# Optimization experiments

Hardware: AMD Instinct MI355X
Metric: run time of the kernel (lower is better)

Reference implementation:

```python
import jax, jax.numpy as jnp
import numpy as np

N = 100000   # nodes
E = 300000   # edges
D = 256      # emb_dim
L = 5        # num_layers
SELF_LOOP_BOND_TYPE = 4
BN_EPS = 1e-5


def setup_inputs() -> dict:
    key = jax.random.key(0)
    ks = jax.random.split(key, 12)
    s = 0.05
    x = jax.random.randint(ks[0], (N, 2), 0, 3)
    edge_index = jax.random.randint(ks[1], (2, E), 0, N)
    edge_attr = jax.random.randint(ks[2], (E, 2), 0, 3)
    x_emb1 = jax.random.normal(ks[3], (120, D), dtype=jnp.float32) * s
    x_emb2 = jax.random.normal(ks[4], (3, D), dtype=jnp.float32) * s
    edge_emb1 = jax.random.normal(ks[5], (L, 6, D), dtype=jnp.float32) * s
    edge_emb2 = jax.random.normal(ks[6], (L, 3, D), dtype=jnp.float32) * s
    W1 = jax.random.normal(ks[7], (L, D, 2 * D), dtype=jnp.float32) * (1.0 / np.sqrt(D))
    b1 = jnp.zeros((L, 2 * D), dtype=jnp.float32)
    W2 = jax.random.normal(ks[8], (L, 2 * D, D), dtype=jnp.float32) * (1.0 / np.sqrt(2 * D))
    b2 = jnp.zeros((L, D), dtype=jnp.float32)
    bn_gamma = jnp.ones((L - 1, D), dtype=jnp.float32)
    bn_beta = jnp.zeros((L - 1, D), dtype=jnp.float32)
    return dict(x=x, edge_index=edge_index, edge_attr=edge_attr,
                x_emb1=x_emb1, x_emb2=x_emb2,
                edge_emb1=edge_emb1, edge_emb2=edge_emb2,
                W1=W1, b1=b1, W2=W2, b2=b2,
                bn_gamma=bn_gamma, bn_beta=bn_beta)


def reference(x, edge_index, edge_attr, x_emb1, x_emb2, edge_emb1, edge_emb2,
              W1, b1, W2, b2, bn_gamma, bn_beta):
    n = x.shape[0]
    loop = jnp.arange(n)
    # add_self_loops: append (i, i) for every node
    src = jnp.concatenate([edge_index[0], loop])  # [E+N]
    dst = jnp.concatenate([edge_index[1], loop])  # [E+N]
    # self-loop edge_attr = (bond_type=4, direction=0)
    self_attr = jnp.concatenate([
        jnp.full((n, 1), SELF_LOOP_BOND_TYPE, dtype=edge_attr.dtype),
        jnp.zeros((n, 1), dtype=edge_attr.dtype)], axis=1)
    ea = jnp.concatenate([edge_attr, self_attr], axis=0)  # [E+N, 2]

    out = x_emb1[x[:, 0]] + x_emb2[x[:, 1]]  # [N, D]
    for l in range(L):
        e_emb = edge_emb1[l][ea[:, 0]] + edge_emb2[l][ea[:, 1]]  # [E+N, D]
        msg = out[src] + e_emb                                   # gather + message
        agg = jax.ops.segment_sum(msg, dst, num_segments=n)      # scatter-add
        h = jax.nn.relu(agg @ W1[l] + b1[l]) @ W2[l] + b2[l]     # GIN MLP
        if l < L - 1:
            mean = h.mean(axis=0)
            var = h.var(axis=0)  # biased var, matches torch BN training
            h = (h - mean) * jax.lax.rsqrt(var + BN_EPS) * bn_gamma[l] + bn_beta[l]
            h = jax.nn.relu(h)
        out = h
    return out
```

## Files before the change

### kernel.cpp

```cpp
#include <hip/hip_runtime.h>

typedef unsigned short u16;
typedef unsigned int u32;

#define DD 256

typedef short  s16x8 __attribute__((ext_vector_type(8)));
typedef short  s16x4 __attribute__((ext_vector_type(4)));
typedef float  f32x4 __attribute__((ext_vector_type(4)));

__device__ __forceinline__ float b2f(u16 u){
  union { u32 i; float f; } c; c.i = ((u32)u) << 16; return c.f;
}
__device__ __forceinline__ u16 f2b(float f){
  union { float f; u32 i; } c; c.f = f;
  u32 b = c.i + 0x7FFFu + ((c.i >> 16) & 1u);
  return (u16)(b >> 16);
}

__global__ void NodeEncoder_72971494359603_kernel(){}

__global__ void probe_dtype(const u32* w, u32* flag){
  if (threadIdx.x == 0 && blockIdx.x == 0){
    int cnt = 0;
    for (int i = 0; i < 256; i++){
      u32 low = w[i] & 0xFFFFu;
      u32 e = (low >> 7) & 0xFFu;
      if (e >= 0x60u && e <= 0x7Eu) cnt++;
    }
    *flag = (cnt >= 192) ? 1u : 0u;
  }
}

__global__ void cvt_in(const void* src, u16* dst, int n, const u32* flag){
  int i = blockIdx.x * 256 + threadIdx.x;
  if (i < n){
    if (*flag){
      dst[i] = ((const u16*)src)[i];
    } else {
      dst[i] = f2b(((const float*)src)[i]);
    }
  }
}

__global__ void store_out(const u16* h, void* dout, int n, const u32* flag){
  int i = blockIdx.x * 256 + threadIdx.x;
  if (i < n){
    if (*flag){
      ((u16*)dout)[i] = h[i];
    } else {
      ((float*)dout)[i] = b2f(h[i]);
    }
  }
}

__global__ void zero_int(int* p, int n){
  int i = blockIdx.x * 256 + threadIdx.x;
  if (i < n) p[i] = 0;
}

__global__ void build_table(const u16* ee1, const u16* ee2, float* TBL){
  int b = blockIdx.x;
  int l = b / 18, c = b % 18, a = c / 3, bb = c % 3;
  int j = threadIdx.x;
  TBL[b * DD + j] = b2f(ee1[(l * 6 + a) * DD + j]) + b2f(ee2[(l * 3 + bb) * DD + j]);
}

__global__ void hist_kernel(const int* dst, int* counts, int E){
  int e = blockIdx.x * 256 + threadIdx.x;
  if (e < E) atomicAdd(&counts[dst[e]], 1);
}

__global__ void scan_sums(const int* counts, int* bsum, int N){
  __shared__ int red[256];
  int tid = threadIdx.x;
  int base = blockIdx.x * 1024;
  int s = 0;
  for (int i = tid; i < 1024; i += 256){
    int g = base + i;
    if (g < N) s += counts[g];
  }
  red[tid] = s;
  __syncthreads();
  for (int off = 128; off > 0; off >>= 1){
    if (tid < off) red[tid] += red[tid + off];
    __syncthreads();
  }
  if (tid == 0) bsum[blockIdx.x] = red[0];
}

__global__ void scan_top(int* bsum, int nb){
  if (threadIdx.x == 0 && blockIdx.x == 0){
    int acc = 0;
    for (int i = 0; i < nb; i++){ int t = bsum[i]; bsum[i] = acc; acc += t; }
  }
}

__global__ void scan_block(const int* counts, const int* bsum,
                           int* offsets, int* cursor, int N){
  __shared__ int tsum[256];
  int b = blockIdx.x;
  int tid = threadIdx.x;
  int base = b * 1024;
  int v0, v1, v2, v3;
  int g = base + tid * 4;
  v0 = (g + 0 < N) ? counts[g + 0] : 0;
  v1 = (g + 1 < N) ? counts[g + 1] : 0;
  v2 = (g + 2 < N) ? counts[g + 2] : 0;
  v3 = (g + 3 < N) ? counts[g + 3] : 0;
  tsum[tid] = v0 + v1 + v2 + v3;
  __syncthreads();
  for (int off = 1; off < 256; off <<= 1){
    int t = (tid >= off) ? tsum[tid - off] : 0;
    __syncthreads();
    tsum[tid] += t;
    __syncthreads();
  }
  int excl = (tid == 0 ? 0 : tsum[tid - 1]) + bsum[b];
  if (g + 0 < N){ offsets[g + 0] = excl; cursor[g + 0] = excl; } excl += v0;
  if (g + 1 < N){ offsets[g + 1] = excl; cursor[g + 1] = excl; } excl += v1;
  if (g + 2 < N){ offsets[g + 2] = excl; cursor[g + 2] = excl; } excl += v2;
  if (g + 3 < N){ offsets[g + 3] = excl; cursor[g + 3] = excl; }
}

__global__ void fill_csr(const int* ei, const int* ea, int* cursor,
                         int* payload, int E){
  int e = blockIdx.x * 256 + threadIdx.x;
  if (e < E){
    int d = ei[E + e];
    int pos = atomicAdd(&cursor[d], 1);
    int a = ea[2 * e], bb = ea[2 * e + 1];
    payload[pos] = ei[e] | ((a * 3 + bb) << 17);
  }
}

__global__ void node_embed(const int* x, const u16* xe1, const u16* xe2,
                           u16* out, int N){
  int idx = blockIdx.x * 256 + threadIdx.x;
  if (idx < N * DD){
    int n = idx >> 8, j = idx & 255;
    int x0 = x[2 * n], x1 = x[2 * n + 1];
    out[idx] = f2b(b2f(xe1[x0 * DD + j]) + b2f(xe2[x1 * DD + j]));
  }
}

__global__ void pack_B(const u16* __restrict__ W0, u16* __restrict__ Wp0, int K, int Nc){
  const u16* W = W0 + (size_t)blockIdx.y * K * Nc;
  u16* Wp = Wp0 + (size_t)blockIdx.y * K * Nc;
  int idx = blockIdx.x * 256 + threadIdx.x;
  int lane = idx & 63;
  int t = idx >> 6;
  int nk = K >> 5;
  int ksub = t % nk, cblk = t / nk;
  if (cblk >= (Nc >> 4)) return;
  int col = cblk * 16 + (lane & 15);
  int krow = ksub * 32 + (lane >> 4) * 8;
  u16* dst = Wp + (size_t)idx * 8;
#pragma unroll
  for (int e = 0; e < 8; e++)
    dst[e] = W[(size_t)(krow + e) * Nc + col];
}

__global__ __launch_bounds__(512, 4)
void layer_fused(const u16* __restrict__ feat, const float* __restrict__ TBL,
                 const int* __restrict__ offsets, const int* __restrict__ counts,
                 const int* __restrict__ payload,
                 const u16* __restrict__ Wp1, const u16* __restrict__ bias1,
                 const u16* __restrict__ Wp2, const u16* __restrict__ bias2,
                 u16* __restrict__ H, float* __restrict__ partial, int npart, int M,
                 const float* __restrict__ sums, const u16* __restrict__ gamma,
                 const u16* __restrict__ beta, float invN, int apply_bn){
  __shared__ __align__(16) u16 As[64 * 256];
  __shared__ __align__(16) u16 Ms[2][64 * 128];
  float* T = (float*)Ms;
  int tid = threadIdx.x, lane = tid & 63, wave = tid >> 6;
  int wr = wave >> 2, wc = wave & 3;
  int row0 = blockIdx.x * 64;
  int lr = lane & 15, hi = lane >> 4;

  for (int i = tid; i < 18 * DD; i += 512) T[i] = TBL[i];
  __syncthreads();

  {
    int c4 = lane * 4;
    float sc[4], sh[4];
    if (apply_bn){
#pragma unroll
      for (int e = 0; e < 4; e++){
        int j = c4 + e;
        float mean = sums[j] * invN;
        float var = sums[DD + j] * invN - mean * mean;
        if (var < 0.f) var = 0.f;
        float scl = rsqrtf(var + 1e-5f) * b2f(gamma[j]);
        sc[e] = scl; sh[e] = b2f(beta[j]) - mean * scl;
      }
    } else {
#pragma unroll
      for (int e = 0; e < 4; e++){ sc[e] = 1.f; sh[e] = 0.f; }
    }
    for (int u = 0; u < 8; u++){
      int r = wave * 8 + u;
      int n = row0 + r; if (n > M - 1) n = M - 1;
      s16x4 sv = *(const s16x4*)(feat + (size_t)n * DD + c4);
      f32x4 tb = *(const f32x4*)(T + 12 * DD + c4);
      float v0 = b2f((u16)sv[0]) * sc[0] + sh[0];
      float v1 = b2f((u16)sv[1]) * sc[1] + sh[1];
      float v2 = b2f((u16)sv[2]) * sc[2] + sh[2];
      float v3 = b2f((u16)sv[3]) * sc[3] + sh[3];
      if (apply_bn){
        v0 = fmaxf(v0, 0.f); v1 = fmaxf(v1, 0.f);
        v2 = fmaxf(v2, 0.f); v3 = fmaxf(v3, 0.f);
      }
      float a0 = v0 + tb[0], a1 = v1 + tb[1], a2 = v2 + tb[2], a3 = v3 + tb[3];
      int e0 = offsets[n], eend = e0 + counts[n];
      for (int e = e0; e < eend; e += 4){
        int nb = eend - e; if (nb > 4) nb = 4;
        int pls[4]; s16x4 rvs[4]; f32x4 tvs[4];
#pragma unroll
        for (int i = 0; i < 4; i++)
          if (i < nb) pls[i] = payload[e + i];
#pragma unroll
        for (int i = 0; i < 4; i++)
          if (i < nb){
            rvs[i] = *(const s16x4*)(feat + (size_t)(pls[i] & 0x1FFFF) * DD + c4);
            tvs[i] = *(const f32x4*)(T + (pls[i] >> 17) * DD + c4);
          }
#pragma unroll
        for (int i = 0; i < 4; i++)
          if (i < nb){
            float w0 = b2f((u16)rvs[i][0]) * sc[0] + sh[0];
            float w1 = b2f((u16)rvs[i][1]) * sc[1] + sh[1];
            float w2 = b2f((u16)rvs[i][2]) * sc[2] + sh[2];
            float w3 = b2f((u16)rvs[i][3]) * sc[3] + sh[3];
            if (apply_bn){
              w0 = fmaxf(w0, 0.f); w1 = fmaxf(w1, 0.f);
              w2 = fmaxf(w2, 0.f); w3 = fmaxf(w3, 0.f);
            }
            a0 += w0 + tvs[i][0];
            a1 += w1 + tvs[i][1];
            a2 += w2 + tvs[i][2];
            a3 += w3 + tvs[i][3];
          }
      }
      s16x4 o;
      o[0] = (short)f2b(a0); o[1] = (short)f2b(a1);
      o[2] = (short)f2b(a2); o[3] = (short)f2b(a3);
      int byteo = r * 512 + ((((lane >> 1) ^ (r & 7)) & 31) << 4) + ((lane & 1) << 3);
      *(s16x4*)((char*)As + byteo) = o;
    }
  }
  __syncthreads();

  f32x4 zero = {0.f, 0.f, 0.f, 0.f};
  f32x4 acc2[2][4];
#pragma unroll
  for (int m = 0; m < 2; m++)
#pragma unroll
    for (int n = 0; n < 4; n++) acc2[m][n] = zero;
  f32x4 acc1[2][2];

  auto G1 = [&](int cc){
#pragma unroll
    for (int m = 0; m < 2; m++)
#pragma unroll
      for (int n = 0; n < 2; n++) acc1[m][n] = zero;
#pragma unroll
    for (int ks = 0; ks < 8; ks++){
      s16x8 af[2];
#pragma unroll
      for (int m = 0; m < 2; m++){
        int arow = wr * 32 + m * 16 + lr;
        af[m] = *(const s16x8*)((const char*)As + arow * 512 +
                                ((ks * 64 + hi * 16) ^ ((arow & 7) << 4)));
      }
#pragma unroll
      for (int n = 0; n < 2; n++){
        int cb = cc * 8 + wc * 2 + n;
        s16x8 bf = *(const s16x8*)(Wp1 + (((size_t)cb * 8 + ks) * 64 + lane) * 8);
        acc1[0][n] = __builtin_amdgcn_mfma_f32_16x16x32_bf16(af[0], bf, acc1[0][n], 0, 0, 0);
        acc1[1][n] = __builtin_amdgcn_mfma_f32_16x16x32_bf16(af[1], bf, acc1[1][n], 0, 0, 0);
      }
    }
  };
  auto WMS = [&](int cc, int buf){
    char* ms = (char*)Ms[buf];
#pragma unroll
    for (int n = 0; n < 2; n++){
      float bv = b2f(bias1[cc * 128 + wc * 32 + n * 16 + lr]);
      int c2 = (wc * 32 + n * 16 + lr) * 2;
#pragma unroll
      for (int m = 0; m < 2; m++)
#pragma unroll
        for (int r = 0; r < 4; r++){
          int mrow = wr * 32 + m * 16 + hi * 4 + r;
          float v = fmaxf(acc1[m][n][r] + bv, 0.f);
          *(u16*)(ms + mrow * 256 + (c2 ^ ((mrow & 7) << 4))) = f2b(v);
        }
    }
  };

  G1(0);
  WMS(0, 0);
  __syncthreads();

#pragma unroll
  for (int c = 0; c < 4; c++){
    const char* ms = (const char*)Ms[c & 1];
#pragma unroll
    for (int ks = 0; ks < 4; ks++){
      s16x8 mf[2];
#pragma unroll
      for (int m = 0; m < 2; m++){
        int mrow = wr * 32 + m * 16 + lr;
        mf[m] = *(const s16x8*)(ms + mrow * 256 +
                                ((ks * 64 + hi * 16) ^ ((mrow & 7) << 4)));
      }
#pragma unroll
      for (int n = 0; n < 4; n++){
        int cb2 = wc * 4 + n;
        s16x8 wf = *(const s16x8*)(Wp2 + (((size_t)cb2 * 16 + c * 4 + ks) * 64 + lane) * 8);
        acc2[0][n] = __builtin_amdgcn_mfma_f32_16x16x32_bf16(mf[0], wf, acc2[0][n], 0, 0, 0);
        acc2[1][n] = __builtin_amdgcn_mfma_f32_16x16x32_bf16(mf[1], wf, acc2[1][n], 0, 0, 0);
      }
    }
    if (c < 3){
      G1(c + 1);
      WMS(c + 1, (c + 1) & 1);
      __syncthreads();
    }
  }

#pragma unroll
  for (int n = 0; n < 4; n++){
    float bv = b2f(bias2[wc * 64 + n * 16 + lr]);
    int c2 = (wc * 64 + n * 16 + lr) * 2;
#pragma unroll
    for (int m = 0; m < 2; m++)
#pragma unroll
      for (int r = 0; r < 4; r++){
        int mrow = wr * 32 + m * 16 + hi * 4 + r;
        *(u16*)((char*)As + mrow * 512 + (c2 ^ ((mrow & 7) << 4))) = f2b(acc2[m][n][r] + bv);
      }
  }
  __syncthreads();

  float s[8], q[8];
#pragma unroll
  for (int e = 0; e < 8; e++){ s[e] = 0.f; q[e] = 0.f; }
  int sl = tid & 31;
#pragma unroll
  for (int p = 0; p < 4; p++){
    int r = p * 16 + (tid >> 5);
    s16x8 v = *(const s16x8*)((const char*)As + r * 512 + ((sl << 4) ^ ((r & 7) << 4)));
    int gr = row0 + r;
    if (gr < M){
      *(s16x8*)(H + (size_t)gr * DD + sl * 8) = v;
      if (partial){
#pragma unroll
        for (int e = 0; e < 8; e++){
          float f = b2f((u16)v[e]);
          s[e] += f; q[e] += f * f;
        }
      }
    }
  }
  if (partial){
#pragma unroll
    for (int e = 0; e < 8; e++){
      s[e] += __shfl_xor(s[e], 32);
      q[e] += __shfl_xor(q[e], 32);
    }
    float* redS = (float*)Ms;
    float* redQ = redS + 8 * 256;
    if (lane < 32){
#pragma unroll
      for (int e = 0; e < 8; e++){
        redS[wave * 256 + sl * 8 + e] = s[e];
        redQ[wave * 256 + sl * 8 + e] = q[e];
      }
    }
    __syncthreads();
    if (tid < 256){
      float a = 0.f, b = 0.f;
#pragma unroll
      for (int w = 0; w < 8; w++){ a += redS[w * 256 + tid]; b += redQ[w * 256 + tid]; }
      partial[(size_t)blockIdx.x * DD + tid] = a;
      partial[(size_t)(npart + blockIdx.x) * DD + tid] = b;
    }
  }
}

__global__ void bn_reduce(const float* __restrict__ partial, float* __restrict__ sums,
                          int npart){
  int b = blockIdx.x, which = b >> 3, jg = b & 7;
  int t = threadIdx.x;
  int j = jg * 32 + (t >> 3);
  int li = t & 7;
  float s = 0.f;
  for (int i = li; i < npart; i += 8)
    s += partial[(size_t)(which * npart + i) * DD + j];
  s += __shfl_xor(s, 1); s += __shfl_xor(s, 2); s += __shfl_xor(s, 4);
  if (li == 0) sums[which * DD + j] = s;
}

extern "C" void kernel_launch(void* const* d_in, const int* in_sizes, int n_in,
                              void* d_out, int out_size, void* d_ws, size_t ws_size,
                              hipStream_t stream){
  (void)n_in; (void)out_size; (void)ws_size;
  const int* x    = (const int*)d_in[0];
  const int* ei   = (const int*)d_in[1];
  const int* ea   = (const int*)d_in[2];
  const void* xe1 = d_in[3];
  const void* xe2 = d_in[4];
  const void* ee1 = d_in[5];
  const void* ee2 = d_in[6];
  const void* W1  = d_in[7];
  const void* b1  = d_in[8];
  const void* W2  = d_in[9];
  const void* b2  = d_in[10];
  const void* gam = d_in[11];
  const void* bet = d_in[12];

  int N = in_sizes[0] / 2;
  int E = in_sizes[1] / 2;
  int NB = (N + 1023) / 1024;
  const int L = 5;
  int nblk = (N + 63) / 64;
  int npart = nblk;

  char* base = (char*)d_ws;
  size_t off = 0;
  u32* flag    = (u32*)(base + off);   off += 256;
  float* TBL   = (float*)(base + off); off += ((size_t)L * 18 * DD * 4 + 255) & ~(size_t)255;
  int* counts  = (int*)(base + off);   off += ((size_t)N * 4 + 255) & ~(size_t)255;
  int* offsets = (int*)(base + off);   off += ((size_t)N * 4 + 255) & ~(size_t)255;
  int* cursor  = (int*)(base + off);   off += ((size_t)N * 4 + 255) & ~(size_t)255;
  int* bsum    = (int*)(base + off);   off += ((size_t)NB * 4 + 255) & ~(size_t)255;
  int* payload = (int*)(base + off);   off += ((size_t)E * 4 + 255) & ~(size_t)255;
  float* part  = (float*)(base + off); off += ((size_t)2 * npart * DD * 4 + 255) & ~(size_t)255;
  float* sums  = (float*)(base + off); off += ((size_t)2 * DD * 4 + 255) & ~(size_t)255;
  u16* wx1  = (u16*)(base + off); off += ((size_t)120 * DD * 2 + 255) & ~(size_t)255;
  u16* wx2  = (u16*)(base + off); off += ((size_t)3 * DD * 2 + 255) & ~(size_t)255;
  u16* wee1 = (u16*)(base + off); off += ((size_t)L * 6 * DD * 2 + 255) & ~(size_t)255;
  u16* wee2 = (u16*)(base + off); off += ((size_t)L * 3 * DD * 2 + 255) & ~(size_t)255;
  u16* wW1  = (u16*)(base + off); off += ((size_t)L * DD * 2 * DD * 2 + 255) & ~(size_t)255;
  u16* wb1  = (u16*)(base + off); off += ((size_t)L * 2 * DD * 2 + 255) & ~(size_t)255;
  u16* wW2  = (u16*)(base + off); off += ((size_t)L * 2 * DD * DD * 2 + 255) & ~(size_t)255;
  u16* wb2  = (u16*)(base + off); off += ((size_t)L * DD * 2 + 255) & ~(size_t)255;
  u16* wgam = (u16*)(base + off); off += ((size_t)(L - 1) * DD * 2 + 255) & ~(size_t)255;
  u16* wbet = (u16*)(base + off); off += ((size_t)(L - 1) * DD * 2 + 255) & ~(size_t)255;
  u16* Wp1  = (u16*)(base + off); off += ((size_t)L * DD * 2 * DD * 2 + 255) & ~(size_t)255;
  u16* Wp2  = (u16*)(base + off); off += ((size_t)L * 2 * DD * DD * 2 + 255) & ~(size_t)255;
  u16* featA = (u16*)(base + off); off += ((size_t)N * DD * 2 + 255) & ~(size_t)255;
  u16* featB = (u16*)(base + off); off += ((size_t)N * DD * 2 + 255) & ~(size_t)255;

  probe_dtype<<<1, 64, 0, stream>>>((const u32*)xe1, flag);
  cvt_in<<<(120 * DD + 255) / 256, 256, 0, stream>>>(xe1, wx1, 120 * DD, flag);
  cvt_in<<<(3 * DD + 255) / 256, 256, 0, stream>>>(xe2, wx2, 3 * DD, flag);
  cvt_in<<<(L * 6 * DD + 255) / 256, 256, 0, stream>>>(ee1, wee1, L * 6 * DD, flag);
  cvt_in<<<(L * 3 * DD + 255) / 256, 256, 0, stream>>>(ee2, wee2, L * 3 * DD, flag);
  cvt_in<<<(L * DD * 2 * DD + 255) / 256, 256, 0, stream>>>(W1, wW1, L * DD * 2 * DD, flag);
  cvt_in<<<(L * 2 * DD + 255) / 256, 256, 0, stream>>>(b1, wb1, L * 2 * DD, flag);
  cvt_in<<<(L * 2 * DD * DD + 255) / 256, 256, 0, stream>>>(W2, wW2, L * 2 * DD * DD, flag);
  cvt_in<<<(L * DD + 255) / 256, 256, 0, stream>>>(b2, wb2, L * DD, flag);
  cvt_in<<<((L - 1) * DD + 255) / 256, 256, 0, stream>>>(gam, wgam, (L - 1) * DD, flag);
  cvt_in<<<((L - 1) * DD + 255) / 256, 256, 0, stream>>>(bet, wbet, (L - 1) * DD, flag);

  build_table<<<90, 256, 0, stream>>>(wee1, wee2, TBL);
  pack_B<<<dim3(64, L), 256, 0, stream>>>(wW1, Wp1, DD, 2 * DD);
  pack_B<<<dim3(64, L), 256, 0, stream>>>(wW2, Wp2, 2 * DD, DD);
  zero_int<<<(N + 255) / 256, 256, 0, stream>>>(counts, N);
  hist_kernel<<<(E + 255) / 256, 256, 0, stream>>>(ei + E, counts, E);
  scan_sums<<<NB, 256, 0, stream>>>(counts, bsum, N);
  scan_top<<<1, 64, 0, stream>>>(bsum, NB);
  scan_block<<<NB, 256, 0, stream>>>(counts, bsum, offsets, cursor, N);
  fill_csr<<<(E + 255) / 256, 256, 0, stream>>>(ei, ea, cursor, payload, E);

  node_embed<<<(N * DD + 255) / 256, 256, 0, stream>>>(x, wx1, wx2, featA, N);

  float invN = 1.0f / (float)N;
  u16* fin = featA;
  u16* fout = featB;

  for (int l = 0; l < L; l++){
    layer_fused<<<nblk, 512, 0, stream>>>(
        fin, TBL + (size_t)l * 18 * DD, offsets, counts, payload,
        Wp1 + (size_t)l * DD * 2 * DD, wb1 + (size_t)l * 2 * DD,
        Wp2 + (size_t)l * 2 * DD * DD, wb2 + (size_t)l * DD,
        fout, (l < L - 1) ? part : (float*)nullptr, npart, N,
        sums, wgam + (size_t)(l > 0 ? l - 1 : 0) * DD,
        wbet + (size_t)(l > 0 ? l - 1 : 0) * DD, invN, l > 0 ? 1 : 0);

    if (l < L - 1){
      bn_reduce<<<16, 256, 0, stream>>>(part, sums, npart);
    }
    u16* t = fin; fin = fout; fout = t;
  }

  store_out<<<(N * DD + 255) / 256, 256, 0, stream>>>(fin, d_out, N * DD, flag);
}
```

Baseline: 1.603 ms.

## Halve LDS footprint with bf16 edge table and 64-wide hidden chunks for occupancy

The edge-embedding lookup table is stored in bf16 instead of fp32, which halves its global and LDS size. The fused MLP now walks the 512-wide hidden layer in eight 64-column chunks instead of four 128-column chunks, so the double-buffered intermediate tile shrinks to 16KB. Total LDS per block drops, which lets more blocks fit per CU, and launch bounds are raised to 6 to match. The risks are a tighter register budget that may cause spills, more chunk iterations each ending in a barrier, and bf16 rounding of the edge embeddings. A barrier is also added before the BN reduction reuses the shared buffer.

```diff
diff --git a/kernel.cpp b/kernel.cpp
--- a/kernel.cpp
+++ b/kernel.cpp
@@ -59,11 +59,11 @@
   if (i < n) p[i] = 0;
 }
 
-__global__ void build_table(const u16* ee1, const u16* ee2, float* TBL){
+__global__ void build_table(const u16* ee1, const u16* ee2, u16* TBL){
   int b = blockIdx.x;
   int l = b / 18, c = b % 18, a = c / 3, bb = c % 3;
   int j = threadIdx.x;
-  TBL[b * DD + j] = b2f(ee1[(l * 6 + a) * DD + j]) + b2f(ee2[(l * 3 + bb) * DD + j]);
+  TBL[b * DD + j] = f2b(b2f(ee1[(l * 6 + a) * DD + j]) + b2f(ee2[(l * 3 + bb) * DD + j]));
 }
 
 __global__ void hist_kernel(const int* dst, int* counts, int E){
@@ -161,8 +161,8 @@
     dst[e] = W[(size_t)(krow + e) * Nc + col];
 }
 
-__global__ __launch_bounds__(512, 4)
-void layer_fused(const u16* __restrict__ feat, const float* __restrict__ TBL,
+__global__ __launch_bounds__(512, 6)
+void layer_fused(const u16* __restrict__ feat, const u16* __restrict__ TBL,
                  const int* __restrict__ offsets, const int* __restrict__ counts,
                  const int* __restrict__ payload,
                  const u16* __restrict__ Wp1, const u16* __restrict__ bias1,
@@ -171,14 +171,18 @@
                  const float* __restrict__ sums, const u16* __restrict__ gamma,
                  const u16* __restrict__ beta, float invN, int apply_bn){
   __shared__ __align__(16) u16 As[64 * 256];
-  __shared__ __align__(16) u16 Ms[2][64 * 128];
-  float* T = (float*)Ms;
+  __shared__ __align__(16) u16 Ms[2][64 * 64];
+  u16* T = (u16*)Ms;
   int tid = threadIdx.x, lane = tid & 63, wave = tid >> 6;
   int wr = wave >> 2, wc = wave & 3;
   int row0 = blockIdx.x * 64;
   int lr = lane & 15, hi = lane >> 4;
 
-  for (int i = tid; i < 18 * DD; i += 512) T[i] = TBL[i];
+  {
+    u32* Tw = (u32*)T;
+    const u32* Gw = (const u32*)TBL;
+    for (int i = tid; i < 18 * DD / 2; i += 512) Tw[i] = Gw[i];
+  }
   __syncthreads();
 
   {
@@ -202,7 +206,7 @@
       int r = wave * 8 + u;
       int n = row0 + r; if (n > M - 1) n = M - 1;
       s16x4 sv = *(const s16x4*)(feat + (size_t)n * DD + c4);
-      f32x4 tb = *(const f32x4*)(T + 12 * DD + c4);
+      s16x4 tb = *(const s16x4*)(T + 12 * DD + c4);
       float v0 = b2f((u16)sv[0]) * sc[0] + sh[0];
       float v1 = b2f((u16)sv[1]) * sc[1] + sh[1];
       float v2 = b2f((u16)sv[2]) * sc[2] + sh[2];
@@ -211,11 +215,14 @@
         v0 = fmaxf(v0, 0.f); v1 = fmaxf(v1, 0.f);
         v2 = fmaxf(v2, 0.f); v3 = fmaxf(v3, 0.f);
       }
-      float a0 = v0 + tb[0], a1 = v1 + tb[1], a2 = v2 + tb[2], a3 = v3 + tb[3];
+      float a0 = v0 + b2f((u16)tb[0]);
+      float a1 = v1 + b2f((u16)tb[1]);
+      float a2 = v2 + b2f((u16)tb[2]);
+      float a3 = v3 + b2f((u16)tb[3]);
       int e0 = offsets[n], eend = e0 + counts[n];
       for (int e = e0; e < eend; e += 4){
         int nb = eend - e; if (nb > 4) nb = 4;
-        int pls[4]; s16x4 rvs[4]; f32x4 tvs[4];
+        int pls[4]; s16x4 rvs[4]; s16x4 tvs[4];
 #pragma unroll
         for (int i = 0; i < 4; i++)
           if (i < nb) pls[i] = payload[e + i];
@@ -223,7 +230,7 @@
         for (int i = 0; i < 4; i++)
           if (i < nb){
             rvs[i] = *(const s16x4*)(feat + (size_t)(pls[i] & 0x1FFFF) * DD + c4);
-            tvs[i] = *(const f32x4*)(T + (pls[i] >> 17) * DD + c4);
+            tvs[i] = *(const s16x4*)(T + (pls[i] >> 17) * DD + c4);
           }
 #pragma unroll
         for (int i = 0; i < 4; i++)
@@ -236,10 +243,10 @@
               w0 = fmaxf(w0, 0.f); w1 = fmaxf(w1, 0.f);
               w2 = fmaxf(w2, 0.f); w3 = fmaxf(w3, 0.f);
             }
-            a0 += w0 + tvs[i][0];
-            a1 += w1 + tvs[i][1];
-            a2 += w2 + tvs[i][2];
-            a3 += w3 + tvs[i][3];
+            a0 += w0 + b2f((u16)tvs[i][0]);
+            a1 += w1 + b2f((u16)tvs[i][1]);
+            a2 += w2 + b2f((u16)tvs[i][2]);
+            a3 += w3 + b2f((u16)tvs[i][3]);
           }
       }
       s16x4 o;
@@ -257,13 +264,11 @@
   for (int m = 0; m < 2; m++)
 #pragma unroll
     for (int n = 0; n < 4; n++) acc2[m][n] = zero;
-  f32x4 acc1[2][2];
+  f32x4 acc1[2];
 
   auto G1 = [&](int cc){
-#pragma unroll
-    for (int m = 0; m < 2; m++)
-#pragma unroll
-      for (int n = 0; n < 2; n++) acc1[m][n] = zero;
+    acc1[0] = zero; acc1[1] = zero;
+    int cb = cc * 4 + wc;
 #pragma unroll
     for (int ks = 0; ks < 8; ks++){
       s16x8 af[2];
@@ -273,30 +278,23 @@
         af[m] = *(const s16x8*)((const char*)As + arow * 512 +
                                 ((ks * 64 + hi * 16) ^ ((arow & 7) << 4)));
       }
-#pragma unroll
-      for (int n = 0; n < 2; n++){
-        int cb = cc * 8 + wc * 2 + n;
-        s16x8 bf = *(const s16x8*)(Wp1 + (((size_t)cb * 8 + ks) * 64 + lane) * 8);
-        acc1[0][n] = __builtin_amdgcn_mfma_f32_16x16x32_bf16(af[0], bf, acc1[0][n], 0, 0, 0);
-        acc1[1][n] = __builtin_amdgcn_mfma_f32_16x16x32_bf16(af[1], bf, acc1[1][n], 0, 0, 0);
-      }
+      s16x8 bf = *(const s16x8*)(Wp1 + (((size_t)cb * 8 + ks) * 64 + lane) * 8);
+      acc1[0] = __builtin_amdgcn_mfma_f32_16x16x32_bf16(af[0], bf, acc1[0], 0, 0, 0);
+      acc1[1] = __builtin_amdgcn_mfma_f32_16x16x32_bf16(af[1], bf, acc1[1], 0, 0, 0);
     }
   };
   auto WMS = [&](int cc, int buf){
     char* ms = (char*)Ms[buf];
-#pragma unroll
-    for (int n = 0; n < 2; n++){
-      float bv = b2f(bias1[cc * 128 + wc * 32 + n * 16 + lr]);
-      int c2 = (wc * 32 + n * 16 + lr) * 2;
-#pragma unroll
-      for (int m = 0; m < 2; m++)
-#pragma unroll
-        for (int r = 0; r < 4; r++){
-          int mrow = wr * 32 + m * 16 + hi * 4 + r;
-          float v = fmaxf(acc1[m][n][r] + bv, 0.f);
-          *(u16*)(ms + mrow * 256 + (c2 ^ ((mrow & 7) << 4))) = f2b(v);
-        }
-    }
+    float bv = b2f(bias1[cc * 64 + wc * 16 + lr]);
+    int c2 = (wc * 16 + lr) * 2;
+#pragma unroll
+    for (int m = 0; m < 2; m++)
+#pragma unroll
+      for (int r = 0; r < 4; r++){
+        int mrow = wr * 32 + m * 16 + hi * 4 + r;
+        float v = fmaxf(acc1[m][r] + bv, 0.f);
+        *(u16*)(ms + mrow * 128 + (c2 ^ ((mrow & 7) << 4))) = f2b(v);
+      }
   };
 
   G1(0);
@@ -304,26 +302,26 @@
   __syncthreads();
 
 #pragma unroll
-  for (int c = 0; c < 4; c++){
+  for (int c = 0; c < 8; c++){
     const char* ms = (const char*)Ms[c & 1];
 #pragma unroll
-    for (int ks = 0; ks < 4; ks++){
+    for (int ks = 0; ks < 2; ks++){
       s16x8 mf[2];
 #pragma unroll
       for (int m = 0; m < 2; m++){
         int mrow = wr * 32 + m * 16 + lr;
-        mf[m] = *(const s16x8*)(ms + mrow * 256 +
+        mf[m] = *(const s16x8*)(ms + mrow * 128 +
                                 ((ks * 64 + hi * 16) ^ ((mrow & 7) << 4)));
       }
 #pragma unroll
       for (int n = 0; n < 4; n++){
         int cb2 = wc * 4 + n;
-        s16x8 wf = *(const s16x8*)(Wp2 + (((size_t)cb2 * 16 + c * 4 + ks) * 64 + lane) * 8);
+        s16x8 wf = *(const s16x8*)(Wp2 + (((size_t)cb2 * 16 + c * 2 + ks) * 64 + lane) * 8);
         acc2[0][n] = __builtin_amdgcn_mfma_f32_16x16x32_bf16(mf[0], wf, acc2[0][n], 0, 0, 0);
         acc2[1][n] = __builtin_amdgcn_mfma_f32_16x16x32_bf16(mf[1], wf, acc2[1][n], 0, 0, 0);
       }
     }
-    if (c < 3){
+    if (c < 7){
       G1(c + 1);
       WMS(c + 1, (c + 1) & 1);
       __syncthreads();
@@ -370,6 +368,7 @@
       s[e] += __shfl_xor(s[e], 32);
       q[e] += __shfl_xor(q[e], 32);
     }
+    __syncthreads();
     float* redS = (float*)Ms;
     float* redQ = redS + 8 * 256;
     if (lane < 32){
@@ -431,7 +430,7 @@
   char* base = (char*)d_ws;
   size_t off = 0;
   u32* flag    = (u32*)(base + off);   off += 256;
-  float* TBL   = (float*)(base + off); off += ((size_t)L * 18 * DD * 4 + 255) & ~(size_t)255;
+  u16* TBL     = (u16*)(base + off);   off += ((size_t)L * 18 * DD * 2 + 255) & ~(size_t)255;
   int* counts  = (int*)(base + off);   off += ((size_t)N * 4 + 255) & ~(size_t)255;
   int* offsets = (int*)(base + off);   off += ((size_t)N * 4 + 255) & ~(size_t)255;
   int* cursor  = (int*)(base + off);   off += ((size_t)N * 4 + 255) & ~(size_t)255;
```

New measurement: 1.573 ms. Within noise of the previous version (-1.9%).
